# Performance work log

Measured on AMD Instinct MI355X. Metric: run time of the kernel, lower is better.

## Reference

```python
import jax, jax.numpy as jnp
import numpy as np

NUM_HEADS = 16
HEAD_DIM = 64
HIDDEN = NUM_HEADS * HEAD_DIM


def setup_inputs() -> dict:
    key = jax.random.key(0)
    ks = jax.random.split(key, 10)
    B, S = 4, 4096
    return {
        "x": jax.random.normal(ks[0], (B, S, HIDDEN), dtype=jnp.float32),
        "Wq": jax.random.normal(ks[1], (HIDDEN, HIDDEN), dtype=jnp.float32) * 0.02,
        "bq": jax.random.normal(ks[2], (HIDDEN,), dtype=jnp.float32) * 0.02,
        "Wk": jax.random.normal(ks[3], (HIDDEN, HIDDEN), dtype=jnp.float32) * 0.02,
        "bk": jax.random.normal(ks[4], (HIDDEN,), dtype=jnp.float32) * 0.02,
        "Wv": jax.random.normal(ks[5], (HIDDEN, HIDDEN), dtype=jnp.float32) * 0.02,
        "bv": jax.random.normal(ks[6], (HIDDEN,), dtype=jnp.float32) * 0.02,
        "Wo": jax.random.normal(ks[7], (HIDDEN, HIDDEN), dtype=jnp.float32) * 0.02,
        "bo": jax.random.normal(ks[8], (HIDDEN,), dtype=jnp.float32) * 0.02,
        "scale": jax.random.normal(ks[9], (HEAD_DIM,), dtype=jnp.float32),
    }


def reference(x, Wq, bq, Wk, bk, Wv, bv, Wo, bo, scale):
    B, S, _ = x.shape
    # Linear layers (torch Linear: y = x @ W.T + b)
    q = (x @ Wq.T + bq).reshape(B, S, NUM_HEADS, HEAD_DIM)
    k = (x @ Wk.T + bk).reshape(B, S, NUM_HEADS, HEAD_DIM)
    v = (x @ Wv.T + bv).reshape(B, S, NUM_HEADS, HEAD_DIM)
    q = q * scale  # per-head-dim learned scale
    # NOTE: original torch code never moves heads to dim 1, so matmul
    # contracts over head_dim, giving per-token head-to-head scores [B,S,H,H].
    inv_sqrt_d = 1.0 / np.sqrt(HEAD_DIM).astype(np.float32)
    scores = jnp.einsum('bshd,bstd->bsht', q, k) * inv_sqrt_d  # [B,S,H,H]
    attn = jax.nn.softmax(scores, axis=-1)
    out = jnp.einsum('bsht,bstd->bshd', attn, v).reshape(B, S, HIDDEN)
    return out @ Wo.T + bo
```

## Files before the change

### kernel.cpp

```cpp
#include <hip/hip_runtime.h>
#include <hip/hip_fp16.h>
#include <cstdint>
#include <cstddef>

#define NHEAD 16
#define HDIM  64
#define HID   1024

using f16x8 = __attribute__((ext_vector_type(8))) _Float16;
using f32x4 = __attribute__((ext_vector_type(4))) float;

typedef const __attribute__((address_space(1))) unsigned int* gq_t;
typedef __attribute__((address_space(3))) unsigned int* lq_t;

__global__ void cvt_f32_f16(const float* __restrict__ in, _Float16* __restrict__ out, int n8) {
    for (int i = blockIdx.x * blockDim.x + threadIdx.x; i < n8; i += gridDim.x * blockDim.x) {
        const float4* p = (const float4*)(in + (size_t)i * 8);
        float4 a = p[0], b = p[1];
        f16x8 o;
        o[0] = (_Float16)a.x; o[1] = (_Float16)a.y; o[2] = (_Float16)a.z; o[3] = (_Float16)a.w;
        o[4] = (_Float16)b.x; o[5] = (_Float16)b.y; o[6] = (_Float16)b.z; o[7] = (_Float16)b.w;
        *(f16x8*)(out + (size_t)i * 8) = o;
    }
}


#define VMCNT4  asm volatile("s_waitcnt vmcnt(4)" ::: "memory")
#define VMCNT0  asm volatile("s_waitcnt vmcnt(0)" ::: "memory")
#define LGKM0   asm volatile("s_waitcnt lgkmcnt(0)" ::: "memory")
#define BAR     __builtin_amdgcn_s_barrier()

#define READ_A(MH) { \
    const int base = buf * 32768 + (MH) * 8192 + (wm * 64) * 64; \
    _Pragma("unroll") for (int mi = 0; mi < 4; ++mi) { \
        const int rl = mi * 16 + l15; \
        _Pragma("unroll") for (int kk = 0; kk < 2; ++kk) { \
            const int slot = (kk * 4 + g) ^ l7; \
            a[mi][kk] = *(const f16x8*)&lds[base + rl * 64 + slot * 8]; \
        } } }

#define READ_B(NH, BREG) { \
    const int base = buf * 32768 + 16384 + (NH) * 8192 + (wn * 32) * 64; \
    _Pragma("unroll") for (int ni = 0; ni < 2; ++ni) { \
        const int rl = ni * 16 + l15; \
        _Pragma("unroll") for (int kk = 0; kk < 2; ++kk) { \
            const int slot = (kk * 4 + g) ^ l7; \
            BREG[ni][kk] = *(const f16x8*)&lds[base + rl * 64 + slot * 8]; \
        } } }

#define STAGE_A(T, MH) if ((T) < NT) { \
    const int bufS = (T) & 1; \
    _Pragma("unroll") for (int s = 0; s < 2; ++s) { \
        const int rho = s * 64 + wid * 8 + r_in; \
        const int r = ((rho >> 6) << 7) + (MH) * 64 + (rho & 63); \
        const int sg = s_l ^ r_in; \
        const _Float16* src = A + (size_t)(m0 + r) * K + (size_t)(T) * 64 + sg * 8; \
        _Float16* dst = (_Float16*)&lds[bufS * 32768 + (MH) * 8192 + (s * 64 + wid * 8) * 64]; \
        __builtin_amdgcn_global_load_lds((gq_t)(const void*)src, (lq_t)(void*)dst, 16, 0, 0); \
    } }

#define STAGE_B(T, NH) if ((T) < NT) { \
    const int bufS = (T) & 1; \
    _Pragma("unroll") for (int s = 0; s < 2; ++s) { \
        const int rho = s * 64 + wid * 8 + r_in; \
        const int r = ((rho >> 5) << 6) + (NH) * 32 + (rho & 31); \
        const int sg = s_l ^ r_in; \
        const _Float16* src = Bw + (size_t)(n0 + r) * K + (size_t)(T) * 64 + sg * 8; \
        _Float16* dst = (_Float16*)&lds[bufS * 32768 + 16384 + (NH) * 8192 + (s * 64 + wid * 8) * 64]; \
        __builtin_amdgcn_global_load_lds((gq_t)(const void*)src, (lq_t)(void*)dst, 16, 0, 0); \
    } }

#define MFMA_QUAD(MO, NO, BREG) \
    __builtin_amdgcn_s_setprio(1); \
    _Pragma("unroll") for (int mi = 0; mi < 4; ++mi) \
    _Pragma("unroll") for (int ni = 0; ni < 2; ++ni) \
    _Pragma("unroll") for (int kk = 0; kk < 2; ++kk) \
        acc[(MO) + mi][(NO) + ni] = __builtin_amdgcn_mfma_f32_16x16x32_f16( \
            a[mi][kk], BREG[ni][kk], acc[(MO) + mi][(NO) + ni], 0, 0, 0); \
    __builtin_amdgcn_s_setprio(0);

template <typename OutT>
__global__ __launch_bounds__(512, 2)
void gemm_bt8(const _Float16* __restrict__ A, const _Float16* __restrict__ Bw,
              const float* __restrict__ bias, OutT* __restrict__ C,
              int M, int N, int K)
{
    __shared__ _Float16 lds[65536];

    const int tid  = threadIdx.x;
    const int lane = tid & 63;
    const int wid  = tid >> 6;
    const int wm   = wid >> 2;
    const int wn   = wid & 3;
    const int m0   = blockIdx.y * 256;
    const int n0   = blockIdx.x * 256;
    const int NT   = K >> 6;

    const int l15  = lane & 15;
    const int l7   = lane & 7;
    const int g    = lane >> 4;
    const int r_in = lane >> 3;
    const int s_l  = lane & 7;

    f32x4 acc[8][4] = {};
    f16x8 a[4][2], b0[2][2], b1[2][2];

    STAGE_A(0, 0); STAGE_B(0, 0); STAGE_B(0, 1); STAGE_A(0, 1);
    STAGE_A(1, 0); STAGE_B(1, 0);
    VMCNT4;
    BAR;

    for (int t = 0; t < NT; ++t) {
        const int buf = t & 1;

        READ_A(0); READ_B(0, b0);
        STAGE_B(t + 1, 1);
        BAR;
        LGKM0; __builtin_amdgcn_sched_barrier(0);
        MFMA_QUAD(0, 0, b0);
        BAR;

        READ_B(1, b1);
        STAGE_A(t + 1, 1);
        BAR;
        LGKM0; __builtin_amdgcn_sched_barrier(0);
        MFMA_QUAD(0, 2, b1);
        BAR;

        READ_A(1);
        STAGE_A(t + 2, 0);
        BAR;
        LGKM0; __builtin_amdgcn_sched_barrier(0);
        MFMA_QUAD(4, 0, b0);
        BAR;

        STAGE_B(t + 2, 0);
        if (t == NT - 2) { VMCNT0; } else { VMCNT4; }
        BAR;
        MFMA_QUAD(4, 2, b1);
        BAR;
    }

    #pragma unroll
    for (int an = 0; an < 4; ++an) {
        const int col = n0 + wn * 64 + (an >> 1) * 32 + (an & 1) * 16 + l15;
        const float bv = bias[col];
        #pragma unroll
        for (int am = 0; am < 8; ++am) {
            const int rowb = m0 + wm * 128 + (am >> 2) * 64 + (am & 3) * 16 + (lane >> 4) * 4;
            #pragma unroll
            for (int q = 0; q < 4; ++q) {
                const float val = acc[am][an][q] + bv;
                C[(size_t)(rowb + q) * N + col] = (OutT)val;
            }
        }
    }
}

__global__ __launch_bounds__(128, 2)
void attn_kernel(const _Float16* __restrict__ qkv, const float* __restrict__ scale,
                 _Float16* __restrict__ out)
{
    __shared__ _Float16 kv[8][2048];
    __shared__ float sc[64];

    const int tid  = threadIdx.x;
    const int tok0 = blockIdx.x * 8;

    if (tid < 64) sc[tid] = scale[tid];

    #pragma unroll
    for (int it = 0; it < 16; ++it) {
        const int vid = tid + it * 128;
        const int tok = vid >> 8;
        const int ofs = (vid & 255) * 8;
        *(f16x8*)&kv[tok][ofs] =
            *(const f16x8*)&qkv[(size_t)(tok0 + tok) * 3072 + 1024 + ofs];
    }
    __syncthreads();

    const int tok = tid >> 4;
    const int h   = tid & 15;
    const size_t qbase = (size_t)(tok0 + tok) * 3072 + h * 64;

    float q[64];
    #pragma unroll
    for (int d0 = 0; d0 < 64; d0 += 8) {
        f16x8 qv = *(const f16x8*)&qkv[qbase + d0];
        #pragma unroll
        for (int j = 0; j < 8; ++j) q[d0 + j] = (float)qv[j] * sc[d0 + j];
    }

    float s[16];
    #pragma unroll
    for (int t = 0; t < 16; ++t) {
        float a = 0.f;
        #pragma unroll
        for (int d0 = 0; d0 < 64; d0 += 8) {
            f16x8 kvv = *(const f16x8*)&kv[tok][t * 64 + d0];
            #pragma unroll
            for (int j = 0; j < 8; ++j) a += q[d0 + j] * (float)kvv[j];
        }
        s[t] = a * 0.125f;
    }

    float mx = s[0];
    #pragma unroll
    for (int t = 1; t < 16; ++t) mx = fmaxf(mx, s[t]);
    float sum = 0.f;
    #pragma unroll
    for (int t = 0; t < 16; ++t) { s[t] = __expf(s[t] - mx); sum += s[t]; }
    const float inv = 1.f / sum;

    float o[64] = {};
    #pragma unroll
    for (int t = 0; t < 16; ++t) {
        const float a = s[t] * inv;
        #pragma unroll
        for (int d0 = 0; d0 < 64; d0 += 8) {
            f16x8 vv = *(const f16x8*)&kv[tok][1024 + t * 64 + d0];
            #pragma unroll
            for (int j = 0; j < 8; ++j) o[d0 + j] += a * (float)vv[j];
        }
    }

    #pragma unroll
    for (int d0 = 0; d0 < 64; d0 += 8) {
        f16x8 ov;
        #pragma unroll
        for (int j = 0; j < 8; ++j) ov[j] = (_Float16)o[d0 + j];
        *(f16x8*)&out[(size_t)(tok0 + tok) * 1024 + h * 64 + d0] = ov;
    }
}

extern "C" void kernel_launch(void* const* d_in, const int* in_sizes, int n_in,
                              void* d_out, int out_size, void* d_ws, size_t ws_size,
                              hipStream_t stream)
{
    const float* x     = (const float*)d_in[0];
    const float* Wq    = (const float*)d_in[1];
    const float* bq    = (const float*)d_in[2];
    const float* Wk    = (const float*)d_in[3];
    const float* bk    = (const float*)d_in[4];
    const float* Wv    = (const float*)d_in[5];
    const float* bv    = (const float*)d_in[6];
    const float* Wo    = (const float*)d_in[7];
    const float* bo    = (const float*)d_in[8];
    const float* scale = (const float*)d_in[9];
    float* out = (float*)d_out;

    const int M = in_sizes[0] / HID;

    char* ws = (char*)d_ws;
    _Float16* x16    = (_Float16*)ws;
    _Float16* attn16 = x16;
    _Float16* wqkv16 = (_Float16*)(ws + (size_t)M * HID * 2);
    _Float16* wo16   = wqkv16 + (size_t)3 * HID * HID;
    float*    bqkv   = (float*)(wo16 + (size_t)HID * HID);
    _Float16* qkv16  = (_Float16*)((char*)bqkv + 3 * HID * 4);

    hipMemcpyAsync(bqkv,           bq, HID * 4, hipMemcpyDeviceToDevice, stream);
    hipMemcpyAsync(bqkv + HID,     bk, HID * 4, hipMemcpyDeviceToDevice, stream);
    hipMemcpyAsync(bqkv + 2 * HID, bv, HID * 4, hipMemcpyDeviceToDevice, stream);

    cvt_f32_f16<<<4096, 256, 0, stream>>>(x,  x16,                M * HID / 8);
    cvt_f32_f16<<<1024, 256, 0, stream>>>(Wq, wqkv16,             HID * HID / 8);
    cvt_f32_f16<<<1024, 256, 0, stream>>>(Wk, wqkv16 + HID * HID, HID * HID / 8);
    cvt_f32_f16<<<1024, 256, 0, stream>>>(Wv, wqkv16 + 2*HID*HID, HID * HID / 8);
    cvt_f32_f16<<<1024, 256, 0, stream>>>(Wo, wo16,               HID * HID / 8);

    gemm_bt8<_Float16><<<dim3(3 * HID / 256, M / 256), 512, 0, stream>>>(
        x16, wqkv16, bqkv, qkv16, M, 3 * HID, HID);

    attn_kernel<<<M / 8, 128, 0, stream>>>(qkv16, scale, attn16);

    gemm_bt8<float><<<dim3(HID / 256, M / 256), 512, 0, stream>>>(
        attn16, wo16, bo, out, M, HID, HID);
}
```

Measured before the change: 235.9 us.

## Unroll GEMM main loop by two and restage prefetch schedule; merge weight conversions

```diff
diff --git a/kernel.cpp b/kernel.cpp
--- a/kernel.cpp
+++ b/kernel.cpp
@@ -24,14 +24,33 @@
     }
 }
 
-
+__global__ void cvt_weights(const float* __restrict__ Wq, const float* __restrict__ Wk,
+                            const float* __restrict__ Wv, const float* __restrict__ Wo,
+                            _Float16* __restrict__ wqkv, _Float16* __restrict__ wo, int n8each) {
+    for (int i = blockIdx.x * blockDim.x + threadIdx.x; i < 4 * n8each; i += gridDim.x * blockDim.x) {
+        const int seg = i / n8each;
+        const int off = i - seg * n8each;
+        const float* src = (seg == 0) ? Wq : (seg == 1) ? Wk : (seg == 2) ? Wv : Wo;
+        _Float16* dst = (seg < 3) ? (wqkv + (size_t)seg * HID * HID) : wo;
+        const float4* p = (const float4*)(src + (size_t)off * 8);
+        float4 a = p[0], b = p[1];
+        f16x8 o;
+        o[0] = (_Float16)a.x; o[1] = (_Float16)a.y; o[2] = (_Float16)a.z; o[3] = (_Float16)a.w;
+        o[4] = (_Float16)b.x; o[5] = (_Float16)b.y; o[6] = (_Float16)b.z; o[7] = (_Float16)b.w;
+        *(f16x8*)(dst + (size_t)off * 8) = o;
+    }
+}
+
+
+#define VMCNT6  asm volatile("s_waitcnt vmcnt(6)" ::: "memory")
 #define VMCNT4  asm volatile("s_waitcnt vmcnt(4)" ::: "memory")
 #define VMCNT0  asm volatile("s_waitcnt vmcnt(0)" ::: "memory")
 #define LGKM0   asm volatile("s_waitcnt lgkmcnt(0)" ::: "memory")
+#define LGKM8   asm volatile("s_waitcnt lgkmcnt(8)" ::: "memory")
 #define BAR     __builtin_amdgcn_s_barrier()
 
-#define READ_A(MH) { \
-    const int base = buf * 32768 + (MH) * 8192 + (wm * 64) * 64; \
+#define READ_A(BUF, MH) { \
+    const int base = (BUF) * 32768 + (MH) * 8192 + (wm * 64) * 64; \
     _Pragma("unroll") for (int mi = 0; mi < 4; ++mi) { \
         const int rl = mi * 16 + l15; \
         _Pragma("unroll") for (int kk = 0; kk < 2; ++kk) { \
@@ -39,8 +58,8 @@
             a[mi][kk] = *(const f16x8*)&lds[base + rl * 64 + slot * 8]; \
         } } }
 
-#define READ_B(NH, BREG) { \
-    const int base = buf * 32768 + 16384 + (NH) * 8192 + (wn * 32) * 64; \
+#define READ_B(BUF, NH, BREG) { \
+    const int base = (BUF) * 32768 + 16384 + (NH) * 8192 + (wn * 32) * 64; \
     _Pragma("unroll") for (int ni = 0; ni < 2; ++ni) { \
         const int rl = ni * 16 + l15; \
         _Pragma("unroll") for (int kk = 0; kk < 2; ++kk) { \
@@ -79,6 +98,33 @@
             a[mi][kk], BREG[ni][kk], acc[(MO) + mi][(NO) + ni], 0, 0, 0); \
     __builtin_amdgcn_s_setprio(0);
 
+#define TILE(T, BUF) { \
+     \
+    READ_A(BUF, 0); READ_B(BUF, 0, b0); \
+    STAGE_A((T) + 1, 1); \
+    LGKM8; \
+    BAR; LGKM0; \
+    MFMA_QUAD(0, 0, b0); \
+    BAR; \
+     \
+    READ_B(BUF, 1, b1); \
+    STAGE_A((T) + 2, 0); \
+    BAR; LGKM0; \
+    MFMA_QUAD(0, 2, b1); \
+    BAR; \
+     \
+    READ_A(BUF, 1); \
+    STAGE_B((T) + 2, 0); \
+    BAR; LGKM0; \
+    MFMA_QUAD(4, 0, b0); \
+    BAR; \
+     \
+    STAGE_B((T) + 2, 1); \
+    if ((T) == NT - 2) { VMCNT0; } else { VMCNT6; } \
+    BAR; \
+    MFMA_QUAD(4, 2, b1); \
+    BAR; }
+
 template <typename OutT>
 __global__ __launch_bounds__(512, 2)
 void gemm_bt8(const _Float16* __restrict__ A, const _Float16* __restrict__ Bw,
@@ -106,39 +152,14 @@
     f16x8 a[4][2], b0[2][2], b1[2][2];
 
     STAGE_A(0, 0); STAGE_B(0, 0); STAGE_B(0, 1); STAGE_A(0, 1);
-    STAGE_A(1, 0); STAGE_B(1, 0);
     VMCNT4;
+    STAGE_A(1, 0); STAGE_B(1, 0); STAGE_B(1, 1);
+    VMCNT6;
     BAR;
 
-    for (int t = 0; t < NT; ++t) {
-        const int buf = t & 1;
-
-        READ_A(0); READ_B(0, b0);
-        STAGE_B(t + 1, 1);
-        BAR;
-        LGKM0; __builtin_amdgcn_sched_barrier(0);
-        MFMA_QUAD(0, 0, b0);
-        BAR;
-
-        READ_B(1, b1);
-        STAGE_A(t + 1, 1);
-        BAR;
-        LGKM0; __builtin_amdgcn_sched_barrier(0);
-        MFMA_QUAD(0, 2, b1);
-        BAR;
-
-        READ_A(1);
-        STAGE_A(t + 2, 0);
-        BAR;
-        LGKM0; __builtin_amdgcn_sched_barrier(0);
-        MFMA_QUAD(4, 0, b0);
-        BAR;
-
-        STAGE_B(t + 2, 0);
-        if (t == NT - 2) { VMCNT0; } else { VMCNT4; }
-        BAR;
-        MFMA_QUAD(4, 2, b1);
-        BAR;
+    for (int e = 0; e < NT; e += 2) {
+        TILE(e, 0);
+        TILE(e + 1, 1);
     }
 
     #pragma unroll
@@ -194,14 +215,14 @@
     float s[16];
     #pragma unroll
     for (int t = 0; t < 16; ++t) {
-        float a = 0.f;
+        float acc = 0.f;
         #pragma unroll
         for (int d0 = 0; d0 < 64; d0 += 8) {
             f16x8 kvv = *(const f16x8*)&kv[tok][t * 64 + d0];
             #pragma unroll
-            for (int j = 0; j < 8; ++j) a += q[d0 + j] * (float)kvv[j];
+            for (int j = 0; j < 8; ++j) acc += q[d0 + j] * (float)kvv[j];
         }
-        s[t] = a * 0.125f;
+        s[t] = acc * 0.125f;
     }
 
     float mx = s[0];
@@ -215,12 +236,12 @@
     float o[64] = {};
     #pragma unroll
     for (int t = 0; t < 16; ++t) {
-        const float a = s[t] * inv;
+        const float aw = s[t] * inv;
         #pragma unroll
         for (int d0 = 0; d0 < 64; d0 += 8) {
             f16x8 vv = *(const f16x8*)&kv[tok][1024 + t * 64 + d0];
             #pragma unroll
-            for (int j = 0; j < 8; ++j) o[d0 + j] += a * (float)vv[j];
+            for (int j = 0; j < 8; ++j) o[d0 + j] += aw * (float)vv[j];
         }
     }
 
@@ -263,11 +284,8 @@
     hipMemcpyAsync(bqkv + HID,     bk, HID * 4, hipMemcpyDeviceToDevice, stream);
     hipMemcpyAsync(bqkv + 2 * HID, bv, HID * 4, hipMemcpyDeviceToDevice, stream);
 
-    cvt_f32_f16<<<4096, 256, 0, stream>>>(x,  x16,                M * HID / 8);
-    cvt_f32_f16<<<1024, 256, 0, stream>>>(Wq, wqkv16,             HID * HID / 8);
-    cvt_f32_f16<<<1024, 256, 0, stream>>>(Wk, wqkv16 + HID * HID, HID * HID / 8);
-    cvt_f32_f16<<<1024, 256, 0, stream>>>(Wv, wqkv16 + 2*HID*HID, HID * HID / 8);
-    cvt_f32_f16<<<1024, 256, 0, stream>>>(Wo, wo16,               HID * HID / 8);
+    cvt_f32_f16<<<4096, 256, 0, stream>>>(x, x16, M * HID / 8);
+    cvt_weights<<<2048, 256, 0, stream>>>(Wq, Wk, Wv, Wo, wqkv16, wo16, HID * HID / 8);
 
     gemm_bt8<_Float16><<<dim3(3 * HID / 256, M / 256), 512, 0, stream>>>(
         x16, wqkv16, bqkv, qkv16, M, 3 * HID, HID);
```

After: 224.4 us. 4.9% less time.
